# Optimization experiments

Measured on AMD Instinct MI355X. Metric: run time of the kernel, lower is better.

The kernel has to match this reference:

```python
import jax, jax.numpy as jnp
import numpy as np

N, E, D = 50000, 800000, 256
H1, C1 = 4, 64          # conv1: heads=4, out=64 -> concat dim 256
H2, C2 = 1, 2           # conv2: heads=1, out=2, concat=False
NEG_SLOPE = 0.2
LN_EPS = 1e-5


def _gatv2(x, src, dst, n, Wl, bl, Wr, br, att, bias, concat):
    """PyG GATv2Conv (eval mode, add_self_loops already applied to src/dst)."""
    H, C = att.shape
    xl = (x @ Wl + bl).reshape(n, H, C)   # source-side transform (x_j)
    xr = (x @ Wr + br).reshape(n, H, C)   # target-side transform (x_i)
    e = xl[src] + xr[dst]                 # [E, H, C]
    e = jnp.where(e > 0, e, NEG_SLOPE * e)          # LeakyReLU(0.2)
    logits = jnp.einsum('ehc,hc->eh', e, att)       # [E, H]
    m = jax.ops.segment_max(logits, dst, num_segments=n)
    a = jnp.exp(logits - m[dst])
    denom = jax.ops.segment_sum(a, dst, num_segments=n)
    alpha = a / denom[dst]                          # segment softmax over in-edges
    msg = xl[src] * alpha[:, :, None]               # [E, H, C]
    out = jax.ops.segment_sum(msg, dst, num_segments=n)  # [n, H, C]
    if concat:
        return out.reshape(n, H * C) + bias
    return out.mean(axis=1) + bias


def _layernorm(x, g, b):
    mu = x.mean(-1, keepdims=True)
    var = ((x - mu) ** 2).mean(-1, keepdims=True)
    return (x - mu) * jax.lax.rsqrt(var + LN_EPS) * g + b


def setup_inputs() -> dict:
    key = jax.random.key(0)
    ks = jax.random.split(key, 20)
    s = 0.05
    HC = H1 * C1
    return {
        'x': jax.random.normal(ks[0], (N, D), jnp.float32),
        'edge_index': jax.random.randint(ks[1], (2, E), 0, N, jnp.int64),
        # conv1 params
        'W1l': jax.random.normal(ks[2], (D, HC), jnp.float32) * s,
        'b1l': jnp.zeros((HC,), jnp.float32),
        'W1r': jax.random.normal(ks[3], (D, HC), jnp.float32) * s,
        'b1r': jnp.zeros((HC,), jnp.float32),
        'att1': jax.random.normal(ks[4], (H1, C1), jnp.float32) * s,
        'bias1': jnp.zeros((HC,), jnp.float32),
        # conv2 params (in = HC, out = 2, 1 head, concat=False)
        'W2l': jax.random.normal(ks[5], (HC, H2 * C2), jnp.float32) * s,
        'b2l': jnp.zeros((H2 * C2,), jnp.float32),
        'W2r': jax.random.normal(ks[6], (HC, H2 * C2), jnp.float32) * s,
        'b2r': jnp.zeros((H2 * C2,), jnp.float32),
        'att2': jax.random.normal(ks[7], (H2, C2), jnp.float32) * s,
        'bias2': jnp.zeros((C2,), jnp.float32),
        # skip Linear(D, HC)
        'Wskip': jax.random.normal(ks[8], (D, HC), jnp.float32) * s,
        'bskip': jnp.zeros((HC,), jnp.float32),
        # LayerNorm(HC)
        'gamma': jnp.ones((HC,), jnp.float32),
        'beta': jnp.zeros((HC,), jnp.float32),
    }


def reference(x, edge_index, W1l, b1l, W1r, b1r, att1, bias1,
              W2l, b2l, W2r, b2r, att2, bias2, Wskip, bskip, gamma, beta):
    n = x.shape[0]
    loops = jnp.arange(n, dtype=edge_index.dtype)  # PyG add_self_loops=True
    src = jnp.concatenate([edge_index[0], loops])
    dst = jnp.concatenate([edge_index[1], loops])
    h = _gatv2(x, src, dst, n, W1l, b1l, W1r, b1r, att1, bias1, True)
    h = h + x @ Wskip + bskip
    h = jax.nn.elu(_layernorm(h, gamma, beta))
    # dropout p=0.3 is identity in eval mode
    return _gatv2(h, src, dst, n, W2l, b2l, W2r, b2r, att2, bias2, False)
```

## Files before the change

kernel.cpp:

```cpp
#include <hip/hip_runtime.h>
#include <hip/hip_fp16.h>

#define NNODES 50000
#define NEDGES 800000
#define CAP    80
#define CAST_BLKS 12500
#define TR_BLKS   192
#define ZERO_BLKS 196

using half8 = __attribute__((ext_vector_type(8))) _Float16;
using half2v = __attribute__((ext_vector_type(2))) _Float16;
using ushort8v = __attribute__((ext_vector_type(8))) unsigned short;
using float4v = __attribute__((ext_vector_type(4))) float;

__device__ __forceinline__ float scrub(float v) {
    if (!(v == v)) return 0.f;
    return fminf(fmaxf(v, -1e30f), 1e30f);
}

__global__ __launch_bounds__(256) void prep_k(
    const float* __restrict__ x, __half* __restrict__ xb,
    const float* __restrict__ W0, const float* __restrict__ W1,
    const float* __restrict__ W2,
    __half* __restrict__ T0, __half* __restrict__ T1, __half* __restrict__ T2,
    int* __restrict__ deg)
{
    __shared__ float tile[32][33];
    int b = blockIdx.x;
    if (b < CAST_BLKS) {
        size_t i = (size_t)b * 256 + threadIdx.x;
        float4 v = ((const float4*)x)[i];
        __half o[4] = {__float2half(v.x), __float2half(v.y),
                       __float2half(v.z), __float2half(v.w)};
        *(uint2*)(xb + 4 * i) = *(uint2*)o;
        return;
    }
    b -= CAST_BLKS;
    if (b < TR_BLKS) {
        int bz = b >> 6, rem = b & 63;
        int bx = rem & 7, by = rem >> 3;
        const float* W = (bz == 0) ? W0 : (bz == 1) ? W1 : W2;
        __half*     T  = (bz == 0) ? T0 : (bz == 1) ? T1 : T2;
        const int r0 = by * 32, c0 = bx * 32;
        const int tc = threadIdx.x & 31, tr = threadIdx.x >> 5;
#pragma unroll
        for (int i = 0; i < 4; i++)
            tile[tr + 8 * i][tc] = W[(size_t)(r0 + tr + 8 * i) * 256 + c0 + tc];
        __syncthreads();
#pragma unroll
        for (int i = 0; i < 4; i++)
            T[(size_t)(c0 + tr + 8 * i) * 256 + r0 + tc] =
                __float2half(tile[tc][tr + 8 * i]);
        return;
    }
    b -= TR_BLKS;
    int i = b * 256 + threadIdx.x;
    if (i < NNODES) deg[i] = 0;
}

__global__ __launch_bounds__(256) void gemm3(
    const __half* __restrict__ A,
    const __half* __restrict__ Bt0, const __half* __restrict__ Bt1,
    const __half* __restrict__ Bt2,
    const float* __restrict__ bias0, const float* __restrict__ bias1,
    const float* __restrict__ bias2, const float* __restrict__ bias2b,
    __half* __restrict__ o0, __half* __restrict__ o1, __half* __restrict__ o2, int M)
{
    __shared__ __half As[64 * 40];
    __shared__ __half Bs0[64 * 40], Bs1[64 * 40], Bs2[64 * 40];
    const int t = threadIdx.x;
    const int lane = t & 63, w = t >> 6;
    const int quad = lane >> 4, r16 = lane & 15;
    const int m0 = blockIdx.x * 64, n0 = blockIdx.y * 64;
    const int lrow = t >> 2, lk = (t & 3) * 8;

    float4v acc[3][4];
#pragma unroll
    for (int j = 0; j < 3; j++)
#pragma unroll
        for (int i = 0; i < 4; i++) acc[j][i] = (float4v){0.f, 0.f, 0.f, 0.f};

    for (int k0 = 0; k0 < 256; k0 += 32) {
        uint4 av = {0u, 0u, 0u, 0u};
        int gm = m0 + lrow;
        if (gm < M) av = *(const uint4*)(A + (size_t)gm * 256 + k0 + lk);
        *(uint4*)(As + lrow * 40 + lk) = av;
        const size_t bo = (size_t)(n0 + lrow) * 256 + k0 + lk;
        *(uint4*)(Bs0 + lrow * 40 + lk) = *(const uint4*)(Bt0 + bo);
        *(uint4*)(Bs1 + lrow * 40 + lk) = *(const uint4*)(Bt1 + bo);
        *(uint4*)(Bs2 + lrow * 40 + lk) = *(const uint4*)(Bt2 + bo);
        __syncthreads();
        half8 a = *(const half8*)(As + (w * 16 + r16) * 40 + quad * 8);
#pragma unroll
        for (int tt = 0; tt < 4; tt++) {
            const int boff = (tt * 16 + r16) * 40 + quad * 8;
            half8 b0v = *(const half8*)(Bs0 + boff);
            acc[0][tt] = __builtin_amdgcn_mfma_f32_16x16x32_f16(a, b0v, acc[0][tt], 0, 0, 0);
            half8 b1v = *(const half8*)(Bs1 + boff);
            acc[1][tt] = __builtin_amdgcn_mfma_f32_16x16x32_f16(a, b1v, acc[1][tt], 0, 0, 0);
            half8 b2v = *(const half8*)(Bs2 + boff);
            acc[2][tt] = __builtin_amdgcn_mfma_f32_16x16x32_f16(a, b2v, acc[2][tt], 0, 0, 0);
        }
        __syncthreads();
    }
#pragma unroll
    for (int tt = 0; tt < 4; tt++) {
        int n = n0 + tt * 16 + r16;
        float bv0 = bias0[n], bv1 = bias1[n], bv2 = bias2[n] + bias2b[n];
#pragma unroll
        for (int j = 0; j < 4; j++) {
            int m = m0 + w * 16 + quad * 4 + j;
            if (m < M) {
                size_t idx = (size_t)m * 256 + n;
                o0[idx] = __float2half(acc[0][tt][j] + bv0);
                o1[idx] = __float2half(acc[1][tt][j] + bv1);
                o2[idx] = __float2half(acc[2][tt][j] + bv2);
            }
        }
    }
}

__global__ void scatter_pad(const int* __restrict__ ei,
                            int* __restrict__ deg, int* __restrict__ csr) {
    __shared__ int stS;
    if (threadIdx.x == 0) {
        int orv = 0;
#pragma unroll
        for (int k = 1; k < 32; k += 2) orv |= ei[k];
        stS = orv ? 1 : 2;
    }
    __syncthreads();
    int st = stS;
    int e = blockIdx.x * 256 + threadIdx.x;
    if (e >= NEDGES) return;
    int s = ei[(size_t)st * e];
    int d = ei[(size_t)st * (NEDGES + e)];
    if ((unsigned)s >= NNODES) s = 0;
    if ((unsigned)d >= NNODES) d = 0;
    int pos = atomicAdd(&deg[d], 1);
    if (pos < CAP) csr[(size_t)d * CAP + pos] = s;
}

__global__ __launch_bounds__(256) void node_conv1(
    const int* __restrict__ deg, const int* __restrict__ csr,
    const __half* __restrict__ xl, const __half* __restrict__ xr_,
    const __half* __restrict__ acc_,
    const float* __restrict__ att,
    const float* __restrict__ g_, const float* __restrict__ bt_,
    const float* __restrict__ W2l, const float* __restrict__ b2l,
    const float* __restrict__ W2r, const float* __restrict__ b2r,
    float* __restrict__ xl2, float* __restrict__ xr2)
{
    const int node = blockIdx.x * 4 + (threadIdx.x >> 6);
    if (node >= NNODES) return;
    const int lane = threadIdx.x & 63;
    const int sub = lane >> 5;
    const int ch0 = ((lane & 31) >> 3) * 64 + (lane & 7) * 8;

    union U8 { ushort8v u; half2v h[4]; };

    half2v atth[4], xrh[4];
    {
        const float4 aA = *(const float4*)(att + ch0);
        const float4 aB = *(const float4*)(att + ch0 + 4);
        atth[0] = (half2v){(_Float16)aA.x, (_Float16)aA.y};
        atth[1] = (half2v){(_Float16)aA.z, (_Float16)aA.w};
        atth[2] = (half2v){(_Float16)aB.x, (_Float16)aB.y};
        atth[3] = (half2v){(_Float16)aB.z, (_Float16)aB.w};
        U8 X; X.u = *(const ushort8v*)((const unsigned short*)xr_ + (size_t)node * 256 + ch0);
#pragma unroll
        for (int i = 0; i < 4; i++) xrh[i] = X.h[i];
    }
    const half2v c02 = (half2v){(_Float16)0.2f, (_Float16)0.2f};

    const char* __restrict__ xlB = (const char*)xl;
    const unsigned offL = (unsigned)(ch0 * 2);
#define ROW8(srcv) (*(const ushort8v*)(xlB + (size_t)((((unsigned)(srcv)) << 9) + offL)))

    int dg = deg[node]; if (dg > CAP) dg = CAP;
    const int* __restrict__ q = csr + (size_t)node * CAP;

    float s = 0.f;
    half2v ah[4];
#pragma unroll
    for (int i = 0; i < 4; i++) ah[i] = (half2v){(_Float16)0.f, (_Float16)0.f};

    int e0 = sub;
    int sv;
    {
        int qi = e0 - 1; if (qi < 0) qi = 0;
        sv = q[qi];
        if (e0 == 0) sv = node;
        if ((unsigned)sv >= NNODES) sv = 0;
    }
    bool val = (e0 <= dg);
    ushort8v row = ROW8(sv);

    const int npair = (dg + 2) >> 1;
    for (int k = 0; k < npair; k++) {
        int en = e0 + 2;
        int sn = q[en - 1];
        if ((unsigned)sn >= NNODES) sn = 0;
        ushort8v rown = ROW8(sn);
        bool valn = (en <= dg);

        U8 cur; cur.u = row;
        half2v p2 = (half2v){(_Float16)0.f, (_Float16)0.f};
#pragma unroll
        for (int i = 0; i < 4; i++) {
            half2v e = cur.h[i] + xrh[i];
            half2v l = e * c02;
            e = __builtin_elementwise_max(e, l);
            p2 = __builtin_elementwise_fma(atth[i], e, p2);
        }
        float part = (float)p2[0] + (float)p2[1];
        part += __shfl_xor(part, 1);
        part += __shfl_xor(part, 2);
        part += __shfl_xor(part, 4);
        float lg = fminf(fmaxf(part, -30.f), 6.f);
        float pe = __expf(lg);
        pe = val ? pe : 0.f;
        s += pe;
        _Float16 peh = (_Float16)pe;
        half2v pe2 = (half2v){peh, peh};
#pragma unroll
        for (int i = 0; i < 4; i++)
            ah[i] = __builtin_elementwise_fma(pe2, cur.h[i], ah[i]);

        row = rown; val = valn; e0 = en;
    }
#undef ROW8

    s += __shfl_xor(s, 32);
#pragma unroll
    for (int i = 0; i < 4; i++) {
        union { half2v h; int b; } cvt; cvt.h = ah[i];
        int ob = __shfl_xor(cvt.b, 32);
        union { int b; half2v h; } o; o.b = ob;
        ah[i] = ah[i] + o.h;
    }

    float D = s;
    if (!(D > 0.f)) D = 1.f;
    float invD = 1.f / D;

    float tot[8];
    {
        U8 au; au.u = *(const ushort8v*)((const unsigned short*)acc_ + (size_t)node * 256 + ch0);
#pragma unroll
        for (int i = 0; i < 4; i++) {
            tot[2*i]   = scrub((float)au.h[i][0] + (float)ah[i][0] * invD);
            tot[2*i+1] = scrub((float)au.h[i][1] + (float)ah[i][1] * invD);
        }
    }

    float s1 = 0.f, s2 = 0.f;
#pragma unroll
    for (int i = 0; i < 8; i++) { s1 += tot[i]; s2 = fmaf(tot[i], tot[i], s2); }
#pragma unroll
    for (int o = 16; o > 0; o >>= 1) { s1 += __shfl_xor(s1, o); s2 += __shfl_xor(s2, o); }
    float mu  = s1 * (1.f / 256.f);
    float var = fmaxf(s2 * (1.f / 256.f) - mu * mu, 0.f);
    float rstd = rsqrtf(var + 1e-5f);

    float gv[8], bv[8];
    {
        const float4 gA = *(const float4*)(g_ + ch0);
        const float4 gB = *(const float4*)(g_ + ch0 + 4);
        const float4 bA = *(const float4*)(bt_ + ch0);
        const float4 bB = *(const float4*)(bt_ + ch0 + 4);
        gv[0]=gA.x; gv[1]=gA.y; gv[2]=gA.z; gv[3]=gA.w;
        gv[4]=gB.x; gv[5]=gB.y; gv[6]=gB.z; gv[7]=gB.w;
        bv[0]=bA.x; bv[1]=bA.y; bv[2]=bA.z; bv[3]=bA.w;
        bv[4]=bB.x; bv[5]=bB.y; bv[6]=bB.z; bv[7]=bB.w;
    }
    float h[8];
#pragma unroll
    for (int i = 0; i < 8; i++) {
        float y = (tot[i] - mu) * rstd * gv[i] + bv[i];
        h[i] = y > 0.f ? y : (__expf(y) - 1.f);
        h[i] = scrub(h[i]);
    }

    float p0 = 0.f, p1 = 0.f, p2 = 0.f, p3 = 0.f;
    {
        const float4* wl = (const float4*)(W2l + ch0 * 2);
        const float4* wr = (const float4*)(W2r + ch0 * 2);
#pragma unroll
        for (int i = 0; i < 4; i++) {
            float4 wlv = wl[i];
            float4 wrv = wr[i];
            p0 = fmaf(h[2*i], wlv.x, p0); p0 = fmaf(h[2*i+1], wlv.z, p0);
            p1 = fmaf(h[2*i], wlv.y, p1); p1 = fmaf(h[2*i+1], wlv.w, p1);
            p2 = fmaf(h[2*i], wrv.x, p2); p2 = fmaf(h[2*i+1], wrv.z, p2);
            p3 = fmaf(h[2*i], wrv.y, p3); p3 = fmaf(h[2*i+1], wrv.w, p3);
        }
    }
#pragma unroll
    for (int o = 16; o > 0; o >>= 1) {
        p0 += __shfl_xor(p0, o); p1 += __shfl_xor(p1, o);
        p2 += __shfl_xor(p2, o); p3 += __shfl_xor(p3, o);
    }
    if (lane == 0) {
        xl2[(size_t)node * 2 + 0] = scrub(p0 + b2l[0]);
        xl2[(size_t)node * 2 + 1] = scrub(p1 + b2l[1]);
        xr2[(size_t)node * 2 + 0] = scrub(p2 + b2r[0]);
        xr2[(size_t)node * 2 + 1] = scrub(p3 + b2r[1]);
    }
}

__global__ __launch_bounds__(256) void node_conv2(
    const int* __restrict__ deg, const int* __restrict__ csr,
    const float* __restrict__ xl2, const float* __restrict__ xr2,
    const float* __restrict__ att2, const float* __restrict__ bias2,
    float* __restrict__ out)
{
    int node = blockIdx.x * 8 + (threadIdx.x >> 5);
    if (node >= NNODES) return;
    int hl = threadIdx.x & 31;
    float a0 = att2[0], a1 = att2[1];
    float2 xr = *(const float2*)(xr2 + (size_t)node * 2);
    int dg = deg[node]; if (dg > CAP) dg = CAP;
    const int* __restrict__ q = csr + (size_t)node * CAP;

    float s = 0.f, o0 = 0.f, o1 = 0.f;
    {
        float2 v = *(const float2*)(xl2 + (size_t)node * 2);
        float e0 = v.x + xr.x; e0 = fmaxf(e0, 0.2f * e0);
        float e1 = v.y + xr.y; e1 = fmaxf(e1, 0.2f * e1);
        float lg = fminf(fmaxf(a0 * e0 + a1 * e1, -60.f), 60.f);
        float pe = (hl == 0) ? __expf(lg) : 0.f;
        s = pe; o0 = pe * v.x; o1 = pe * v.y;
    }
    for (int pb = 0; pb < dg; pb += 32) {
        int p = pb + hl;
        bool valid = p < dg;
        int src = q[p];
        if ((unsigned)src >= NNODES) src = 0;
        float2 v = *(const float2*)(xl2 + (size_t)src * 2);
        float e0 = v.x + xr.x; e0 = fmaxf(e0, 0.2f * e0);
        float e1 = v.y + xr.y; e1 = fmaxf(e1, 0.2f * e1);
        float lg = fminf(fmaxf(a0 * e0 + a1 * e1, -60.f), 60.f);
        float pe = valid ? __expf(lg) : 0.f;
        s += pe; o0 = fmaf(pe, v.x, o0); o1 = fmaf(pe, v.y, o1);
    }
#pragma unroll
    for (int o = 16; o > 0; o >>= 1) {
        s += __shfl_xor(s, o); o0 += __shfl_xor(o0, o); o1 += __shfl_xor(o1, o);
    }
    if (hl == 0) {
        if (!(s > 0.f)) { s = 1.f; o0 = 0.f; o1 = 0.f; }
        float inv = 1.f / s;
        out[(size_t)node * 2 + 0] = scrub(o0 * inv + bias2[0]);
        out[(size_t)node * 2 + 1] = scrub(o1 * inv + bias2[1]);
    }
}

extern "C" void kernel_launch(void* const* d_in, const int* in_sizes, int n_in,
                              void* d_out, int out_size, void* d_ws, size_t ws_size,
                              hipStream_t stream) {
    const float* x     = (const float*)d_in[0];
    const int*   ei    = (const int*)d_in[1];
    const float* W1l   = (const float*)d_in[2];
    const float* b1l   = (const float*)d_in[3];
    const float* W1r   = (const float*)d_in[4];
    const float* b1r   = (const float*)d_in[5];
    const float* att1  = (const float*)d_in[6];
    const float* bias1 = (const float*)d_in[7];
    const float* W2l   = (const float*)d_in[8];
    const float* b2l   = (const float*)d_in[9];
    const float* W2r   = (const float*)d_in[10];
    const float* b2r   = (const float*)d_in[11];
    const float* att2  = (const float*)d_in[12];
    const float* bias2 = (const float*)d_in[13];
    const float* Wsk   = (const float*)d_in[14];
    const float* bsk   = (const float*)d_in[15];
    const float* g_    = (const float*)d_in[16];
    const float* bt_   = (const float*)d_in[17];

    size_t off = 0;
    auto alloc = [&](size_t b) {
        void* p = (char*)d_ws + off;
        off += (b + 255) & ~(size_t)255;
        return p;
    };
    int*    deg  = (int*)alloc((size_t)NNODES * 4);
    int*    csr  = (int*)alloc(((size_t)NNODES * CAP + 256) * 4);
    float*  xl2  = (float*)alloc((size_t)NNODES * 8);
    float*  xr2  = (float*)alloc((size_t)NNODES * 8);
    __half* Wt1l = (__half*)alloc(256 * 256 * 2);
    __half* Wt1r = (__half*)alloc(256 * 256 * 2);
    __half* Wtsk = (__half*)alloc(256 * 256 * 2);
    __half* xb   = (__half*)alloc((size_t)NNODES * 256 * 2);
    __half* xl1  = (__half*)alloc((size_t)NNODES * 256 * 2);
    __half* xr1  = (__half*)alloc((size_t)NNODES * 256 * 2);
    __half* acc1 = (__half*)alloc((size_t)NNODES * 256 * 2);

    prep_k<<<CAST_BLKS + TR_BLKS + ZERO_BLKS, 256, 0, stream>>>(
        x, xb, W1l, W1r, Wsk, Wt1l, Wt1r, Wtsk, deg);

    gemm3<<<dim3((NNODES + 63) / 64, 4), 256, 0, stream>>>(
        xb, Wt1l, Wt1r, Wtsk, b1l, b1r, bsk, bias1, xl1, xr1, acc1, NNODES);

    scatter_pad<<<(NEDGES + 255) / 256, 256, 0, stream>>>(ei, deg, csr);

    node_conv1<<<(NNODES + 3) / 4, 256, 0, stream>>>(deg, csr, xl1, xr1, acc1,
                                                     att1, g_, bt_, W2l, b2l, W2r, b2r,
                                                     xl2, xr2);
    node_conv2<<<(NNODES + 7) / 8, 256, 0, stream>>>(deg, csr, xl2, xr2, att2, bias2,
                                                     (float*)d_out);
}
```

Before: 308.4 us.

## Load MFMA fragments directly from global memory and scatter two edges per thread

The fused three-output GEMM no longer stages A and B tiles through shared memory with barriers. Each wave now reads its half8 fragments straight from global memory in a fully unrolled k-loop, relying on L1/L2 to absorb the reads that the four waves repeat on the same B data. The edge scatter kernel now handles two edges per thread using vectorized int2/int4 loads of the index array, and its grid is halved. The risks are more cache traffic and no row bounds check on A loads in the last partial block, which reads past the end of the input buffer.

Result: slower. 435.6 us (+41.2%).

```diff
diff --git a/kernel.cpp b/kernel.cpp
--- a/kernel.cpp
+++ b/kernel.cpp
@@ -66,13 +66,15 @@
     const float* __restrict__ bias2, const float* __restrict__ bias2b,
     __half* __restrict__ o0, __half* __restrict__ o1, __half* __restrict__ o2, int M)
 {
-    __shared__ __half As[64 * 40];
-    __shared__ __half Bs0[64 * 40], Bs1[64 * 40], Bs2[64 * 40];
     const int t = threadIdx.x;
     const int lane = t & 63, w = t >> 6;
     const int quad = lane >> 4, r16 = lane & 15;
     const int m0 = blockIdx.x * 64, n0 = blockIdx.y * 64;
-    const int lrow = t >> 2, lk = (t & 3) * 8;
+
+    const __half* ap  = A   + (size_t)(m0 + w * 16 + r16) * 256 + quad * 8;
+    const __half* bp0 = Bt0 + (size_t)(n0 + r16) * 256 + quad * 8;
+    const __half* bp1 = Bt1 + (size_t)(n0 + r16) * 256 + quad * 8;
+    const __half* bp2 = Bt2 + (size_t)(n0 + r16) * 256 + quad * 8;
 
     float4v acc[3][4];
 #pragma unroll
@@ -80,29 +82,21 @@
 #pragma unroll
         for (int i = 0; i < 4; i++) acc[j][i] = (float4v){0.f, 0.f, 0.f, 0.f};
 
+#pragma unroll
     for (int k0 = 0; k0 < 256; k0 += 32) {
-        uint4 av = {0u, 0u, 0u, 0u};
-        int gm = m0 + lrow;
-        if (gm < M) av = *(const uint4*)(A + (size_t)gm * 256 + k0 + lk);
-        *(uint4*)(As + lrow * 40 + lk) = av;
-        const size_t bo = (size_t)(n0 + lrow) * 256 + k0 + lk;
-        *(uint4*)(Bs0 + lrow * 40 + lk) = *(const uint4*)(Bt0 + bo);
-        *(uint4*)(Bs1 + lrow * 40 + lk) = *(const uint4*)(Bt1 + bo);
-        *(uint4*)(Bs2 + lrow * 40 + lk) = *(const uint4*)(Bt2 + bo);
-        __syncthreads();
-        half8 a = *(const half8*)(As + (w * 16 + r16) * 40 + quad * 8);
+        half8 a = *(const half8*)(ap + k0);
 #pragma unroll
         for (int tt = 0; tt < 4; tt++) {
-            const int boff = (tt * 16 + r16) * 40 + quad * 8;
-            half8 b0v = *(const half8*)(Bs0 + boff);
-            acc[0][tt] = __builtin_amdgcn_mfma_f32_16x16x32_f16(a, b0v, acc[0][tt], 0, 0, 0);
-            half8 b1v = *(const half8*)(Bs1 + boff);
-            acc[1][tt] = __builtin_amdgcn_mfma_f32_16x16x32_f16(a, b1v, acc[1][tt], 0, 0, 0);
-            half8 b2v = *(const half8*)(Bs2 + boff);
-            acc[2][tt] = __builtin_amdgcn_mfma_f32_16x16x32_f16(a, b2v, acc[2][tt], 0, 0, 0);
+            const size_t ro = (size_t)tt * 16 * 256 + k0;
+            half8 b0 = *(const half8*)(bp0 + ro);
+            acc[0][tt] = __builtin_amdgcn_mfma_f32_16x16x32_f16(a, b0, acc[0][tt], 0, 0, 0);
+            half8 b1 = *(const half8*)(bp1 + ro);
+            acc[1][tt] = __builtin_amdgcn_mfma_f32_16x16x32_f16(a, b1, acc[1][tt], 0, 0, 0);
+            half8 b2 = *(const half8*)(bp2 + ro);
+            acc[2][tt] = __builtin_amdgcn_mfma_f32_16x16x32_f16(a, b2, acc[2][tt], 0, 0, 0);
         }
-        __syncthreads();
-    }
+    }
+
 #pragma unroll
     for (int tt = 0; tt < 4; tt++) {
         int n = n0 + tt * 16 + r16;
@@ -131,14 +125,26 @@
     }
     __syncthreads();
     int st = stS;
-    int e = blockIdx.x * 256 + threadIdx.x;
-    if (e >= NEDGES) return;
-    int s = ei[(size_t)st * e];
-    int d = ei[(size_t)st * (NEDGES + e)];
-    if ((unsigned)s >= NNODES) s = 0;
-    if ((unsigned)d >= NNODES) d = 0;
-    int pos = atomicAdd(&deg[d], 1);
-    if (pos < CAP) csr[(size_t)d * CAP + pos] = s;
+    int e0 = (blockIdx.x * 256 + threadIdx.x) * 2;
+    if (e0 >= NEDGES) return;
+    int s0, s1, d0, d1;
+    if (st == 2) {
+        int4 sv = *(const int4*)(ei + 2 * (size_t)e0);
+        int4 dv = *(const int4*)(ei + 2 * (size_t)(NEDGES + e0));
+        s0 = sv.x; s1 = sv.z; d0 = dv.x; d1 = dv.z;
+    } else {
+        int2 sv = *(const int2*)(ei + e0);
+        int2 dv = *(const int2*)(ei + NEDGES + e0);
+        s0 = sv.x; s1 = sv.y; d0 = dv.x; d1 = dv.y;
+    }
+    if ((unsigned)s0 >= NNODES) s0 = 0;
+    if ((unsigned)d0 >= NNODES) d0 = 0;
+    if ((unsigned)s1 >= NNODES) s1 = 0;
+    if ((unsigned)d1 >= NNODES) d1 = 0;
+    int p0 = atomicAdd(&deg[d0], 1);
+    if (p0 < CAP) csr[(size_t)d0 * CAP + p0] = s0;
+    int p1 = atomicAdd(&deg[d1], 1);
+    if (p1 < CAP) csr[(size_t)d1 * CAP + p1] = s1;
 }
 
 __global__ __launch_bounds__(256) void node_conv1(
@@ -402,7 +408,7 @@
     gemm3<<<dim3((NNODES + 63) / 64, 4), 256, 0, stream>>>(
         xb, Wt1l, Wt1r, Wtsk, b1l, b1r, bsk, bias1, xl1, xr1, acc1, NNODES);
 
-    scatter_pad<<<(NEDGES + 255) / 256, 256, 0, stream>>>(ei, deg, csr);
+    scatter_pad<<<(NEDGES / 2 + 255) / 256, 256, 0, stream>>>(ei, deg, csr);
 
     node_conv1<<<(NNODES + 3) / 4, 256, 0, stream>>>(deg, csr, xl1, xr1, acc1,
                                                      att1, g_, bt_, W2l, b2l, W2r, b2r,
```

## Merge GEMM and edge scatter into one launch so they overlap

Applied to the files above, without the earlier changes.

Folds the three-output GEMM and the edge CSR scatter into a single kernel with a flat grid. Block IDs past the GEMM range run the scatter, so atomic-heavy scatter blocks can run alongside compute-bound GEMM blocks, and one launch is removed. The scatter also now handles two edges per thread with vector loads for either index width. This adds a branch and shared-memory usage to the scatter blocks, which may reduce their occupancy.

After: 313.9 us. About the same (+1.8%).

```diff
diff --git a/kernel.cpp b/kernel.cpp
--- a/kernel.cpp
+++ b/kernel.cpp
@@ -7,6 +7,9 @@
 #define CAST_BLKS 12500
 #define TR_BLKS   192
 #define ZERO_BLKS 196
+#define GEMM_BX   782
+#define GEMM_BLKS (GEMM_BX * 4)
+#define SCAT_BLKS 1563
 
 using half8 = __attribute__((ext_vector_type(8))) _Float16;
 using half2v = __attribute__((ext_vector_type(2))) _Float16;
@@ -58,20 +61,58 @@
     if (i < NNODES) deg[i] = 0;
 }
 
-__global__ __launch_bounds__(256) void gemm3(
+__global__ __launch_bounds__(256) void mega_k(
     const __half* __restrict__ A,
     const __half* __restrict__ Bt0, const __half* __restrict__ Bt1,
     const __half* __restrict__ Bt2,
     const float* __restrict__ bias0, const float* __restrict__ bias1,
     const float* __restrict__ bias2, const float* __restrict__ bias2b,
-    __half* __restrict__ o0, __half* __restrict__ o1, __half* __restrict__ o2, int M)
+    __half* __restrict__ o0, __half* __restrict__ o1, __half* __restrict__ o2,
+    int M,
+    const int* __restrict__ ei, int* __restrict__ deg, int* __restrict__ csr)
 {
     __shared__ __half As[64 * 40];
     __shared__ __half Bs0[64 * 40], Bs1[64 * 40], Bs2[64 * 40];
+
+    int blk = blockIdx.x;
+    if (blk >= GEMM_BLKS) {
+        blk -= GEMM_BLKS;
+        __shared__ int stS;
+        if (threadIdx.x == 0) {
+            int orv = 0;
+#pragma unroll
+            for (int k = 1; k < 32; k += 2) orv |= ei[k];
+            stS = orv ? 1 : 2;
+        }
+        __syncthreads();
+        int st = stS;
+        int e0 = (blk * 256 + threadIdx.x) * 2;
+        if (e0 >= NEDGES) return;
+        int s0, s1, d0, d1;
+        if (st == 2) {
+            int4 sv = *(const int4*)(ei + 2 * (size_t)e0);
+            int4 dv = *(const int4*)(ei + 2 * (size_t)(NEDGES + e0));
+            s0 = sv.x; s1 = sv.z; d0 = dv.x; d1 = dv.z;
+        } else {
+            int2 sv = *(const int2*)(ei + e0);
+            int2 dv = *(const int2*)(ei + NEDGES + e0);
+            s0 = sv.x; s1 = sv.y; d0 = dv.x; d1 = dv.y;
+        }
+        if ((unsigned)s0 >= NNODES) s0 = 0;
+        if ((unsigned)d0 >= NNODES) d0 = 0;
+        if ((unsigned)s1 >= NNODES) s1 = 0;
+        if ((unsigned)d1 >= NNODES) d1 = 0;
+        int p0 = atomicAdd(&deg[d0], 1);
+        if (p0 < CAP) csr[(size_t)d0 * CAP + p0] = s0;
+        int p1 = atomicAdd(&deg[d1], 1);
+        if (p1 < CAP) csr[(size_t)d1 * CAP + p1] = s1;
+        return;
+    }
+
     const int t = threadIdx.x;
     const int lane = t & 63, w = t >> 6;
     const int quad = lane >> 4, r16 = lane & 15;
-    const int m0 = blockIdx.x * 64, n0 = blockIdx.y * 64;
+    const int m0 = (blk >> 2) * 64, n0 = (blk & 3) * 64;
     const int lrow = t >> 2, lk = (t & 3) * 8;
 
     float4v acc[3][4];
@@ -118,27 +159,6 @@
             }
         }
     }
-}
-
-__global__ void scatter_pad(const int* __restrict__ ei,
-                            int* __restrict__ deg, int* __restrict__ csr) {
-    __shared__ int stS;
-    if (threadIdx.x == 0) {
-        int orv = 0;
-#pragma unroll
-        for (int k = 1; k < 32; k += 2) orv |= ei[k];
-        stS = orv ? 1 : 2;
-    }
-    __syncthreads();
-    int st = stS;
-    int e = blockIdx.x * 256 + threadIdx.x;
-    if (e >= NEDGES) return;
-    int s = ei[(size_t)st * e];
-    int d = ei[(size_t)st * (NEDGES + e)];
-    if ((unsigned)s >= NNODES) s = 0;
-    if ((unsigned)d >= NNODES) d = 0;
-    int pos = atomicAdd(&deg[d], 1);
-    if (pos < CAP) csr[(size_t)d * CAP + pos] = s;
 }
 
 __global__ __launch_bounds__(256) void node_conv1(
@@ -399,10 +419,9 @@
     prep_k<<<CAST_BLKS + TR_BLKS + ZERO_BLKS, 256, 0, stream>>>(
         x, xb, W1l, W1r, Wsk, Wt1l, Wt1r, Wtsk, deg);
 
-    gemm3<<<dim3((NNODES + 63) / 64, 4), 256, 0, stream>>>(
-        xb, Wt1l, Wt1r, Wtsk, b1l, b1r, bsk, bias1, xl1, xr1, acc1, NNODES);
-
-    scatter_pad<<<(NEDGES + 255) / 256, 256, 0, stream>>>(ei, deg, csr);
+    mega_k<<<GEMM_BLKS + SCAT_BLKS, 256, 0, stream>>>(
+        xb, Wt1l, Wt1r, Wtsk, b1l, b1r, bsk, bias1, xl1, xr1, acc1, NNODES,
+        ei, deg, csr);
 
     node_conv1<<<(NNODES + 3) / 4, 256, 0, stream>>>(deg, csr, xl1, xr1, acc1,
                                                      att1, g_, bt_, W2l, b2l, W2r, b2r,
```
